# Kernel tuning notes

Hardware: AMD Instinct MI355X
Metric: run time of the kernel (lower is better)

The kernel has to match this reference:

```python
import jax, jax.numpy as jnp
import numpy as np
from jax.ops import segment_sum, segment_max

DIM = 32   # hidden dim (hardcoded in Net)
N = 10000  # nodes
E = 160000 # edges
B = 64     # graphs in batch


def setup_inputs():
    key = jax.random.key(0)
    ks = jax.random.split(key, 16)
    r = lambda k, s: jax.random.normal(k, s, dtype=jnp.float32) * 0.1
    z = lambda s: jnp.zeros(s, jnp.float32)
    return {
        "x": jax.random.normal(ks[0], (N, 1), jnp.float32),
        "edge_attr": jax.random.normal(ks[1], (E, 2), jnp.float32),
        "lin0_w": r(ks[2], (1, DIM)), "lin0_b": z((DIM,)),
        "nn_w1": r(ks[3], (2, 128)), "nn_b1": z((128,)),
        "nn_w2": r(ks[4], (128, DIM * DIM)), "nn_b2": z((DIM * DIM,)),
        "conv_root": r(ks[5], (DIM, DIM)), "conv_bias": z((DIM,)),
        "gru_w_ih": r(ks[6], (DIM, 3 * DIM)), "gru_w_hh": r(ks[7], (DIM, 3 * DIM)),
        "gru_b_ih": z((3 * DIM,)), "gru_b_hh": z((3 * DIM,)),
        "lstm_w_ih": r(ks[8], (2 * DIM, 4 * DIM)), "lstm_w_hh": r(ks[9], (DIM, 4 * DIM)),
        "lstm_b_ih": z((4 * DIM,)), "lstm_b_hh": z((4 * DIM,)),
        "lin1_w": r(ks[10], (2 * DIM, DIM)), "lin1_b": z((DIM,)),
        "lin2_w": r(ks[11], (DIM, 1)), "lin2_b": z((1,)),
        "edge_index": jax.random.randint(ks[12], (2, E), 0, N),
        "batch": jnp.sort(jax.random.randint(ks[13], (N,), 0, B)),
    }


def _forward(x, edge_attr, params, edge_index, batch):
    (lin0_w, lin0_b, nn_w1, nn_b1, nn_w2, nn_b2, conv_root, conv_bias,
     gru_w_ih, gru_w_hh, gru_b_ih, gru_b_hh,
     lstm_w_ih, lstm_w_hh, lstm_b_ih, lstm_b_hh,
     lin1_w, lin1_b, lin2_w, lin2_b) = params
    src, dst = edge_index[0], edge_index[1]
    deg = jnp.maximum(segment_sum(jnp.ones((E,), x.dtype), dst, num_segments=N), 1.0)[:, None]
    # edge-conditioned weight matrices (depend only on edge_attr -> compute once)
    ew = (jax.nn.relu(edge_attr @ nn_w1 + nn_b1) @ nn_w2 + nn_b2).reshape(E, DIM, DIM)

    out = jax.nn.relu(x @ lin0_w + lin0_b)  # (N, DIM)
    h = out                                  # GRU hidden state
    for _ in range(3):
        # NNConv: gather -> per-edge matmul -> scatter-mean, plus root weight + bias
        msg = jnp.einsum('ei,eio->eo', out[src], ew)          # (E, DIM)
        agg = segment_sum(msg, dst, num_segments=N) / deg      # (N, DIM)
        m = jax.nn.relu(agg + out @ conv_root + conv_bias)
        # single GRU step (seq_len = 1)
        gi = m @ gru_w_ih + gru_b_ih
        gh = h @ gru_w_hh + gru_b_hh
        i_r, i_z, i_n = jnp.split(gi, 3, axis=-1)
        h_r, h_z, h_n = jnp.split(gh, 3, axis=-1)
        rg = jax.nn.sigmoid(i_r + h_r)
        zg = jax.nn.sigmoid(i_z + h_z)
        ng = jnp.tanh(i_n + rg * h_n)
        h = (1.0 - zg) * ng + zg * h
        out = h

    # Set2Set pooling, 3 processing steps
    q_star = jnp.zeros((B, 2 * DIM), x.dtype)
    hh = jnp.zeros((B, DIM), x.dtype)
    cc = jnp.zeros((B, DIM), x.dtype)
    for _ in range(3):
        gates = q_star @ lstm_w_ih + lstm_b_ih + hh @ lstm_w_hh + lstm_b_hh
        ig, fg, gg, og = jnp.split(gates, 4, axis=-1)  # torch gate order i,f,g,o
        cc = jax.nn.sigmoid(fg) * cc + jax.nn.sigmoid(ig) * jnp.tanh(gg)
        hh = jax.nn.sigmoid(og) * jnp.tanh(cc)
        q = hh                                          # (B, DIM)
        e = jnp.sum(out * q[batch], axis=-1)            # (N,)
        a = jnp.exp(e - segment_max(e, batch, num_segments=B)[batch])
        a = a / segment_sum(a, batch, num_segments=B)[batch]
        rvec = segment_sum(a[:, None] * out, batch, num_segments=B)  # (B, DIM)
        q_star = jnp.concatenate([q, rvec], axis=-1)

    y = jax.nn.relu(q_star @ lin1_w + lin1_b)
    return (y @ lin2_w + lin2_b).reshape(-1)  # (B,)


def reference(x, edge_attr, lin0_w, lin0_b, nn_w1, nn_b1, nn_w2, nn_b2, conv_root, conv_bias, gru_w_ih, gru_w_hh, gru_b_ih, gru_b_hh, lstm_w_ih, lstm_w_hh, lstm_b_ih, lstm_b_hh, lin1_w, lin1_b, lin2_w, lin2_b, edge_index, batch):
    params = (lin0_w, lin0_b, nn_w1, nn_b1, nn_w2, nn_b2, conv_root, conv_bias,
              gru_w_ih, gru_w_hh, gru_b_ih, gru_b_hh,
              lstm_w_ih, lstm_w_hh, lstm_b_ih, lstm_b_hh,
              lin1_w, lin1_b, lin2_w, lin2_b)
    return _forward(x, edge_attr, params, edge_index, batch)
```

## Files before the change

kernel.cpp:

```cpp
#include <hip/hip_runtime.h>
#include <math.h>

#define NN 10000
#define NE 160000
#define NG 64
#define DIM 32
#define CAP 96

typedef __attribute__((ext_vector_type(8))) short bf16x8;
typedef __attribute__((ext_vector_type(4))) float f32x4;

__device__ __forceinline__ float sigmoidf_(float x) { return 1.f / (1.f + expf(-x)); }

__device__ __forceinline__ unsigned short f2bf(float x) {
    unsigned u = __float_as_uint(x);
    u += 0x7FFF + ((u >> 16) & 1);
    return (unsigned short)(u >> 16);
}
__device__ __forceinline__ float bf2f(unsigned short b) {
    return __uint_as_float(((unsigned)b) << 16);
}

__global__ void k_setup(const float* __restrict__ w2, unsigned short* __restrict__ w2f,
                        const float* __restrict__ x, const float* __restrict__ lw,
                        const float* __restrict__ lb, float* __restrict__ out,
                        const int* __restrict__ batch, int* __restrict__ gstart,
                        const int* __restrict__ ei, const float* __restrict__ ea,
                        int* __restrict__ cursor,
                        int* __restrict__ srt_src, float* __restrict__ srt_ea) {
    int b = blockIdx.x, t = threadIdx.x;
    if (b < 512) {
        int tid = b * 256 + t;
        int h = tid >> 10, rem = tid & 1023, i = rem >> 5, n = rem & 31;
        float v = w2[tid];
        unsigned short hi = f2bf(v);
        unsigned short lo = f2bf(v - bf2f(hi));
        int s = h >> 5, hm = h & 31, q = hm >> 3, j = hm & 7;
        int tile = n >> 4, nn = n & 15, lane = q * 16 + nn;
        int c = (i * 4 + s) * 2 + tile;
        w2f[(c * 2 + 0) * 512 + lane * 8 + j] = hi;
        w2f[(c * 2 + 1) * 512 + lane * 8 + j] = lo;
    } else if (b < 1762) {
        int idx = (b - 512) * 256 + t;
        int n = idx >> 5, d = idx & 31;
        out[idx] = fmaxf(x[n] * lw[d] + lb[d], 0.f);
    } else if (b == 1762) {
        if (t <= NG) {
            int g = t, lo = 0, hi = NN;
            while (lo < hi) { int mid = (lo + hi) >> 1; if (batch[mid] < g) lo = mid + 1; else hi = mid; }
            gstart[g] = lo;
        }
    } else {
        int e = (b - 1763) * 256 + t;
        if (e < NE) {
            int d = ei[NE + e];
            int p = atomicAdd(&cursor[d], 1);
            int pos = d * CAP + p;
            srt_src[pos] = ei[e];
            srt_ea[2 * pos]     = ea[2 * e];
            srt_ea[2 * pos + 1] = ea[2 * e + 1];
        }
    }
}

#define NS 1040
#define PS 8320
__global__ __launch_bounds__(512, 4) void k_conv_gru(
    const int* __restrict__ cursor, const int* __restrict__ srt_src,
    const float* __restrict__ srt_ea,
    const float* __restrict__ w1, const float* __restrict__ b1,
    const unsigned short* __restrict__ w2f, const float* __restrict__ b2,
    const float* __restrict__ out_old,
    float* __restrict__ Sg,
    const float* __restrict__ root, const float* __restrict__ cbias,
    const float* __restrict__ wih, const float* __restrict__ whh,
    const float* __restrict__ bih, const float* __restrict__ bhh,
    float* __restrict__ out_new)
{
    __shared__ __align__(16) unsigned short RB[2 * PS];
    int t = threadIdx.x;
    int wave = t >> 6, lane = t & 63;
    int n0 = blockIdx.x * 8;
    int n = n0 + wave;

    float Racc[64];
    #pragma unroll
    for (int i = 0; i < 64; ++i) Racc[i] = 0.f;
    float sacc = 0.f;

    float w1a0 = w1[lane],      w1c0 = w1[128 + lane],  bb0 = b1[lane];
    float w1a1 = w1[64 + lane], w1c1 = w1[192 + lane],  bb1 = b1[64 + lane];

    int rs = n * CAP;
    int re = rs + cursor[n];
    const float2* eap = (const float2*)srt_ea;

    int p = rs;
    for (; p + 1 < re; p += 2) {
        int s0 = __builtin_amdgcn_readfirstlane(srt_src[p]);
        int s1 = __builtin_amdgcn_readfirstlane(srt_src[p + 1]);
        float2 a0 = eap[p];
        float2 a1 = eap[p + 1];
        const float* o0 = out_old + s0 * DIM;
        const float* o1 = out_old + s1 * DIM;
        float r00 = fmaxf(a0.x * w1a0 + a0.y * w1c0 + bb0, 0.f);
        float r01 = fmaxf(a0.x * w1a1 + a0.y * w1c1 + bb1, 0.f);
        float r10 = fmaxf(a1.x * w1a0 + a1.y * w1c0 + bb0, 0.f);
        float r11 = fmaxf(a1.x * w1a1 + a1.y * w1c1 + bb1, 0.f);
        #pragma unroll
        for (int q = 0; q < 32; ++q) {
            float v0 = o0[q];
            Racc[q]      += r00 * v0;
            Racc[32 + q] += r01 * v0;
        }
        #pragma unroll
        for (int q = 0; q < 32; ++q) {
            float v1 = o1[q];
            Racc[q]      += r10 * v1;
            Racc[32 + q] += r11 * v1;
        }
        if (lane < DIM) sacc += o0[lane] + o1[lane];
    }
    if (p < re) {
        int s0 = __builtin_amdgcn_readfirstlane(srt_src[p]);
        float2 a0 = eap[p];
        const float* o0 = out_old + s0 * DIM;
        float r00 = fmaxf(a0.x * w1a0 + a0.y * w1c0 + bb0, 0.f);
        float r01 = fmaxf(a0.x * w1a1 + a0.y * w1c1 + bb1, 0.f);
        #pragma unroll
        for (int q = 0; q < 32; ++q) {
            float v0 = o0[q];
            Racc[q]      += r00 * v0;
            Racc[32 + q] += r01 * v0;
        }
        if (lane < DIM) sacc += o0[lane];
    }
    if (lane < DIM) Sg[n * DIM + lane] = sacc;

    int quad = lane >> 4;
    int mm = lane & 7;
    unsigned aoff = (unsigned)(mm * NS + wave * 128 + quad * 8);
    f32x4 acc0 = {0.f, 0.f, 0.f, 0.f};
    f32x4 acc1 = {0.f, 0.f, 0.f, 0.f};

    unsigned short* Hw = RB + wave * NS;
    unsigned short* Lw = RB + PS + wave * NS;

    #pragma unroll
    for (int pass = 0; pass < 4; ++pass) {
        if (pass) __syncthreads();
        #pragma unroll
        for (int li = 0; li < 8; ++li) {
            float v0 = Racc[pass * 8 + li];
            float v1 = Racc[32 + pass * 8 + li];
            unsigned short h0 = f2bf(v0);
            unsigned short l0 = f2bf(v0 - bf2f(h0));
            unsigned short h1 = f2bf(v1);
            unsigned short l1 = f2bf(v1 - bf2f(h1));
            Hw[li * 128 + lane] = h0;  Hw[li * 128 + 64 + lane] = h1;
            Lw[li * 128 + lane] = l0;  Lw[li * 128 + 64 + lane] = l1;
        }
        __syncthreads();
        int ig = pass * 8 + wave;
        #pragma unroll
        for (int s = 0; s < 4; ++s) {
            bf16x8 ah = *(const bf16x8*)(RB + aoff + s * 32);
            bf16x8 al = *(const bf16x8*)(RB + PS + aoff + s * 32);
            const unsigned short* bp = w2f + (unsigned)((ig * 4 + s) * 2048 + lane * 8);
            bf16x8 bh0 = *(const bf16x8*)(bp);
            bf16x8 bl0 = *(const bf16x8*)(bp + 512);
            bf16x8 bh1 = *(const bf16x8*)(bp + 1024);
            bf16x8 bl1 = *(const bf16x8*)(bp + 1536);
            acc0 = __builtin_amdgcn_mfma_f32_16x16x32_bf16(ah, bh0, acc0, 0, 0, 0);
            acc0 = __builtin_amdgcn_mfma_f32_16x16x32_bf16(ah, bl0, acc0, 0, 0, 0);
            acc0 = __builtin_amdgcn_mfma_f32_16x16x32_bf16(al, bh0, acc0, 0, 0, 0);
            acc1 = __builtin_amdgcn_mfma_f32_16x16x32_bf16(ah, bh1, acc1, 0, 0, 0);
            acc1 = __builtin_amdgcn_mfma_f32_16x16x32_bf16(ah, bl1, acc1, 0, 0, 0);
            acc1 = __builtin_amdgcn_mfma_f32_16x16x32_bf16(al, bh1, acc1, 0, 0, 0);
        }
    }
    __syncthreads();

    float* part = (float*)RB;
    #pragma unroll
    for (int r = 0; r < 4; ++r) {
        part[((wave * 2 + 0) * 64 + lane) * 4 + r] = acc0[r];
        part[((wave * 2 + 1) * 64 + lane) * 4 + r] = acc1[r];
    }
    __syncthreads();

    if (t < 256) {
        int nb = t >> 5, d = t & 31;
        int nn_ = n0 + nb;
        int base = t & 32;
        int tile = d >> 4, col = d & 15;
        int lidx = (nb >> 2) * 16 + col, reg = nb & 3;
        float aggv = 0.f;
        #pragma unroll
        for (int wv = 0; wv < 8; ++wv)
            aggv += part[((wv * 2 + tile) * 64 + lidx) * 4 + reg];

        float bt = 0.f;
        #pragma unroll 8
        for (int i = 0; i < DIM; ++i) bt += Sg[nn_ * DIM + i] * b2[i * DIM + d];
        int cdeg = cursor[nn_];
        float degf = (float)(cdeg > 0 ? cdeg : 1);
        aggv = (aggv + bt) / degf;

        float x = out_old[nn_ * DIM + d];
        float rootsum = 0.f;
        #pragma unroll 8
        for (int k = 0; k < DIM; ++k)
            rootsum += __shfl(x, base + k) * root[k * DIM + d];
        float m = fmaxf(aggv + rootsum + cbias[d], 0.f);

        float gir = bih[d], giz = bih[DIM + d], gin = bih[2 * DIM + d];
        float ghr = bhh[d], ghz = bhh[DIM + d], ghn = bhh[2 * DIM + d];
        #pragma unroll 4
        for (int k = 0; k < DIM; ++k) {
            float mk = __shfl(m, base + k);
            float hk = __shfl(x, base + k);
            gir += mk * wih[k * 96 + d];
            giz += mk * wih[k * 96 + DIM + d];
            gin += mk * wih[k * 96 + 2 * DIM + d];
            ghr += hk * whh[k * 96 + d];
            ghz += hk * whh[k * 96 + DIM + d];
            ghn += hk * whh[k * 96 + 2 * DIM + d];
        }
        float rg = sigmoidf_(gir + ghr);
        float zg = sigmoidf_(giz + ghz);
        float ng = tanhf(gin + rg * ghn);
        out_new[nn_ * DIM + d] = (1.f - zg) * ng + zg * x;
    }
}

__global__ __launch_bounds__(256) void k_set2set(
    const float* __restrict__ out, const int* __restrict__ gstart,
    const float* __restrict__ wih, const float* __restrict__ whh,
    const float* __restrict__ bih, const float* __restrict__ bhh,
    const float* __restrict__ l1w, const float* __restrict__ l1b,
    const float* __restrict__ l2w, const float* __restrict__ l2b,
    float* __restrict__ ebuf, float* __restrict__ y)
{
    __shared__ float swih[64 * 128];
    __shared__ float swhh[32 * 128];
    __shared__ float sq[2 * DIM];
    __shared__ float shh[DIM], scc[DIM];
    __shared__ float sgates[4 * DIM];
    __shared__ float sacc[8][DIM];
    __shared__ float sredA[4], sredB[4];

    int g = blockIdx.x, t = threadIdx.x;
    {
        const float4* wv = (const float4*)wih;   float4* sv = (float4*)swih;
        for (int i = t; i < 2048; i += 256) sv[i] = wv[i];
        const float4* wv2 = (const float4*)whh;  float4* sv2 = (float4*)swhh;
        for (int i = t; i < 1024; i += 256) sv2[i] = wv2[i];
    }
    if (t < 2 * DIM) sq[t] = 0.f;
    if (t < DIM) { shh[t] = 0.f; scc[t] = 0.f; }
    int ns = gstart[g], ne = gstart[g + 1];
    __syncthreads();

    for (int step = 0; step < 3; ++step) {
        if (t < 128) {
            float acc = bih[t] + bhh[t];
            #pragma unroll 8
            for (int k = 0; k < 2 * DIM; ++k) acc += sq[k] * swih[k * 128 + t];
            #pragma unroll 8
            for (int k = 0; k < DIM; ++k)     acc += shh[k] * swhh[k * 128 + t];
            sgates[t] = acc;
        }
        __syncthreads();
        if (t < DIM) {
            float ig = sigmoidf_(sgates[t]);
            float fg = sigmoidf_(sgates[DIM + t]);
            float gg = tanhf(sgates[2 * DIM + t]);
            float og = sigmoidf_(sgates[3 * DIM + t]);
            float c_new = fg * scc[t] + ig * gg;
            float h_new = og * tanhf(c_new);
            scc[t] = c_new;
            shh[t] = h_new;
            sq[t] = h_new;
        }
        __syncthreads();

        float lmax = -3.0e38f;
        for (int n = ns + t; n < ne; n += 256) {
            const float4* orow = (const float4*)(out + n * DIM);
            float e = 0.f;
            #pragma unroll
            for (int q = 0; q < 8; ++q) {
                float4 o4 = orow[q];
                e += o4.x * shh[4 * q] + o4.y * shh[4 * q + 1]
                   + o4.z * shh[4 * q + 2] + o4.w * shh[4 * q + 3];
            }
            ebuf[n] = e;
            lmax = fmaxf(lmax, e);
        }
        #pragma unroll
        for (int s = 1; s < 64; s <<= 1) lmax = fmaxf(lmax, __shfl_xor(lmax, s));
        if ((t & 63) == 0) sredA[t >> 6] = lmax;
        __syncthreads();
        float M = fmaxf(fmaxf(sredA[0], sredA[1]), fmaxf(sredA[2], sredA[3]));

        float lsum = 0.f;
        for (int n = ns + t; n < ne; n += 256) {
            float v = expf(ebuf[n] - M);
            ebuf[n] = v;
            lsum += v;
        }
        #pragma unroll
        for (int s = 1; s < 64; s <<= 1) lsum += __shfl_xor(lsum, s);
        if ((t & 63) == 0) sredB[t >> 6] = lsum;
        __syncthreads();
        float S = sredB[0] + sredB[1] + sredB[2] + sredB[3];
        float inv = (S > 0.f) ? 1.f / S : 0.f;

        int stp = t >> 5, d = t & 31;
        float racc = 0.f;
        for (int n = ns + stp; n < ne; n += 8)
            racc += ebuf[n] * out[n * DIM + d];
        sacc[stp][d] = racc;
        __syncthreads();
        if (t < DIM) {
            float r = 0.f;
            #pragma unroll
            for (int s = 0; s < 8; ++s) r += sacc[s][t];
            sq[DIM + t] = r * inv;
        }
        __syncthreads();
    }

    if (t < DIM) {
        float h = l1b[t];
        #pragma unroll 8
        for (int k = 0; k < 2 * DIM; ++k) h += sq[k] * l1w[k * DIM + t];
        float v = fmaxf(h, 0.f) * l2w[t];
        #pragma unroll
        for (int s = 1; s < 32; s <<= 1) v += __shfl_xor(v, s);
        if (t == 0) y[g] = v + l2b[0];
    }
}

extern "C" void kernel_launch(void* const* d_in, const int* in_sizes, int n_in,
                              void* d_out, int out_size, void* d_ws, size_t ws_size,
                              hipStream_t stream) {
    const float* x         = (const float*)d_in[0];
    const float* edge_attr = (const float*)d_in[1];
    const float* lin0_w    = (const float*)d_in[2];
    const float* lin0_b    = (const float*)d_in[3];
    const float* nn_w1     = (const float*)d_in[4];
    const float* nn_b1     = (const float*)d_in[5];
    const float* nn_w2     = (const float*)d_in[6];
    const float* nn_b2     = (const float*)d_in[7];
    const float* conv_root = (const float*)d_in[8];
    const float* conv_bias = (const float*)d_in[9];
    const float* gru_w_ih  = (const float*)d_in[10];
    const float* gru_w_hh  = (const float*)d_in[11];
    const float* gru_b_ih  = (const float*)d_in[12];
    const float* gru_b_hh  = (const float*)d_in[13];
    const float* lstm_w_ih = (const float*)d_in[14];
    const float* lstm_w_hh = (const float*)d_in[15];
    const float* lstm_b_ih = (const float*)d_in[16];
    const float* lstm_b_hh = (const float*)d_in[17];
    const float* lin1_w    = (const float*)d_in[18];
    const float* lin1_b    = (const float*)d_in[19];
    const float* lin2_w    = (const float*)d_in[20];
    const float* lin2_b    = (const float*)d_in[21];
    const int*   edge_index= (const int*)d_in[22];
    const int*   batch     = (const int*)d_in[23];
    float* yout = (float*)d_out;

    char* p = (char*)d_ws;
    auto alloc = [&](size_t bytes) { char* r = p; p += (bytes + 255) & ~(size_t)255; return r; };

    int*   cursor = (int*)  alloc(NN * sizeof(int));
    size_t zero_bytes = (size_t)(p - (char*)d_ws);
    int*   gstart    = (int*)  alloc((NG + 1) * sizeof(int));
    int*   srt_src   = (int*)  alloc((size_t)NN * CAP * sizeof(int));
    float* srt_ea    = (float*)alloc((size_t)NN * CAP * 2 * sizeof(float));
    float* outA      = (float*)alloc(NN * DIM * sizeof(float));
    float* outB      = (float*)alloc(NN * DIM * sizeof(float));
    float* Sg        = (float*)alloc(NN * DIM * sizeof(float));
    unsigned short* w2f = (unsigned short*)alloc(262144 * sizeof(unsigned short));
    float* ebuf      = (float*)alloc(NN * sizeof(float));
    (void)ws_size; (void)n_in; (void)in_sizes; (void)out_size;

    hipMemsetAsync(d_ws, 0, zero_bytes, stream);

    k_setup<<<2388, 256, 0, stream>>>(nn_w2, w2f, x, lin0_w, lin0_b, outA, batch, gstart,
                                      edge_index, edge_attr, cursor, srt_src, srt_ea);

    const float* cur = outA;
    float* nxt = outB;
    for (int it = 0; it < 3; ++it) {
        k_conv_gru<<<1250, 512, 0, stream>>>(cursor, srt_src, srt_ea,
                                             nn_w1, nn_b1, w2f, nn_b2,
                                             cur, Sg,
                                             conv_root, conv_bias,
                                             gru_w_ih, gru_w_hh, gru_b_ih, gru_b_hh,
                                             nxt);
        const float* tmp = nxt; nxt = (float*)cur; cur = tmp;
    }
    const float* outF = cur;

    k_set2set<<<NG, 256, 0, stream>>>(outF, gstart,
                                      lstm_w_ih, lstm_w_hh, lstm_b_ih, lstm_b_hh,
                                      lin1_w, lin1_b, lin2_w, lin2_b, ebuf, yout);
}
```

Measured before the change: 327.3 us.

## Split each node's hidden accumulation across two waves, four nodes per block

Each block now handles 4 nodes instead of 8, and two waves share one node, each accumulating half of the 128 hidden units. This halves the per-thread accumulator registers and the shared buffer, which allows a higher launch-bounds occupancy target, and doubles the grid size. In exchange, each neighbor row of out_old is gathered by twice as many waves, and the MFMA tiles now run half-empty (M = 4 rows), so W2 loads are amortized over fewer nodes.

```diff
diff --git a/kernel.cpp b/kernel.cpp
--- a/kernel.cpp
+++ b/kernel.cpp
@@ -64,8 +64,8 @@
 }
 
 #define NS 1040
-#define PS 8320
-__global__ __launch_bounds__(512, 4) void k_conv_gru(
+#define PS 4160
+__global__ __launch_bounds__(512, 6) void k_conv_gru(
     const int* __restrict__ cursor, const int* __restrict__ srt_src,
     const float* __restrict__ srt_ea,
     const float* __restrict__ w1, const float* __restrict__ b1,
@@ -80,19 +80,20 @@
     __shared__ __align__(16) unsigned short RB[2 * PS];
     int t = threadIdx.x;
     int wave = t >> 6, lane = t & 63;
-    int n0 = blockIdx.x * 8;
-    int n = n0 + wave;
-
-    float Racc[64];
+    int n0 = blockIdx.x * 4;
+    int node = n0 + (wave >> 1);
+    int hoff = (wave & 1) * 64;
+
+    float Racc[32];
     #pragma unroll
-    for (int i = 0; i < 64; ++i) Racc[i] = 0.f;
+    for (int i = 0; i < 32; ++i) Racc[i] = 0.f;
     float sacc = 0.f;
 
-    float w1a0 = w1[lane],      w1c0 = w1[128 + lane],  bb0 = b1[lane];
-    float w1a1 = w1[64 + lane], w1c1 = w1[192 + lane],  bb1 = b1[64 + lane];
-
-    int rs = n * CAP;
-    int re = rs + cursor[n];
+    int h = hoff + lane;
+    float w1a = w1[h], w1c = w1[128 + h], bb = b1[h];
+
+    int rs = node * CAP;
+    int re = rs + cursor[node];
     const float2* eap = (const float2*)srt_ea;
 
     int p = rs;
@@ -103,48 +104,33 @@
         float2 a1 = eap[p + 1];
         const float* o0 = out_old + s0 * DIM;
         const float* o1 = out_old + s1 * DIM;
-        float r00 = fmaxf(a0.x * w1a0 + a0.y * w1c0 + bb0, 0.f);
-        float r01 = fmaxf(a0.x * w1a1 + a0.y * w1c1 + bb1, 0.f);
-        float r10 = fmaxf(a1.x * w1a0 + a1.y * w1c0 + bb0, 0.f);
-        float r11 = fmaxf(a1.x * w1a1 + a1.y * w1c1 + bb1, 0.f);
-        #pragma unroll
-        for (int q = 0; q < 32; ++q) {
-            float v0 = o0[q];
-            Racc[q]      += r00 * v0;
-            Racc[32 + q] += r01 * v0;
-        }
-        #pragma unroll
-        for (int q = 0; q < 32; ++q) {
-            float v1 = o1[q];
-            Racc[q]      += r10 * v1;
-            Racc[32 + q] += r11 * v1;
-        }
-        if (lane < DIM) sacc += o0[lane] + o1[lane];
+        float rA = fmaxf(a0.x * w1a + a0.y * w1c + bb, 0.f);
+        float rB = fmaxf(a1.x * w1a + a1.y * w1c + bb, 0.f);
+        #pragma unroll
+        for (int q = 0; q < 32; ++q) Racc[q] += rA * o0[q];
+        #pragma unroll
+        for (int q = 0; q < 32; ++q) Racc[q] += rB * o1[q];
+        if (hoff == 0 && lane < DIM) sacc += o0[lane] + o1[lane];
     }
     if (p < re) {
         int s0 = __builtin_amdgcn_readfirstlane(srt_src[p]);
         float2 a0 = eap[p];
         const float* o0 = out_old + s0 * DIM;
-        float r00 = fmaxf(a0.x * w1a0 + a0.y * w1c0 + bb0, 0.f);
-        float r01 = fmaxf(a0.x * w1a1 + a0.y * w1c1 + bb1, 0.f);
-        #pragma unroll
-        for (int q = 0; q < 32; ++q) {
-            float v0 = o0[q];
-            Racc[q]      += r00 * v0;
-            Racc[32 + q] += r01 * v0;
-        }
-        if (lane < DIM) sacc += o0[lane];
-    }
-    if (lane < DIM) Sg[n * DIM + lane] = sacc;
+        float rA = fmaxf(a0.x * w1a + a0.y * w1c + bb, 0.f);
+        #pragma unroll
+        for (int q = 0; q < 32; ++q) Racc[q] += rA * o0[q];
+        if (hoff == 0 && lane < DIM) sacc += o0[lane];
+    }
+    if (hoff == 0 && lane < DIM) Sg[node * DIM + lane] = sacc;
 
     int quad = lane >> 4;
-    int mm = lane & 7;
+    int mm = lane & 3;
     unsigned aoff = (unsigned)(mm * NS + wave * 128 + quad * 8);
     f32x4 acc0 = {0.f, 0.f, 0.f, 0.f};
     f32x4 acc1 = {0.f, 0.f, 0.f, 0.f};
 
-    unsigned short* Hw = RB + wave * NS;
-    unsigned short* Lw = RB + PS + wave * NS;
+    unsigned short* Hw = RB + (wave >> 1) * NS;
+    unsigned short* Lw = RB + PS + (wave >> 1) * NS;
 
     #pragma unroll
     for (int pass = 0; pass < 4; ++pass) {
@@ -152,13 +138,10 @@
         #pragma unroll
         for (int li = 0; li < 8; ++li) {
             float v0 = Racc[pass * 8 + li];
-            float v1 = Racc[32 + pass * 8 + li];
             unsigned short h0 = f2bf(v0);
             unsigned short l0 = f2bf(v0 - bf2f(h0));
-            unsigned short h1 = f2bf(v1);
-            unsigned short l1 = f2bf(v1 - bf2f(h1));
-            Hw[li * 128 + lane] = h0;  Hw[li * 128 + 64 + lane] = h1;
-            Lw[li * 128 + lane] = l0;  Lw[li * 128 + 64 + lane] = l1;
+            Hw[li * 128 + hoff + lane] = h0;
+            Lw[li * 128 + hoff + lane] = l0;
         }
         __syncthreads();
         int ig = pass * 8 + wave;
@@ -189,16 +172,15 @@
     }
     __syncthreads();
 
-    if (t < 256) {
+    if (t < 128) {
         int nb = t >> 5, d = t & 31;
         int nn_ = n0 + nb;
         int base = t & 32;
         int tile = d >> 4, col = d & 15;
-        int lidx = (nb >> 2) * 16 + col, reg = nb & 3;
         float aggv = 0.f;
         #pragma unroll
         for (int wv = 0; wv < 8; ++wv)
-            aggv += part[((wv * 2 + tile) * 64 + lidx) * 4 + reg];
+            aggv += part[((wv * 2 + tile) * 64 + col) * 4 + nb];
 
         float bt = 0.f;
         #pragma unroll 8
@@ -395,7 +377,7 @@
     const float* cur = outA;
     float* nxt = outB;
     for (int it = 0; it < 3; ++it) {
-        k_conv_gru<<<1250, 512, 0, stream>>>(cursor, srt_src, srt_ea,
+        k_conv_gru<<<2500, 512, 0, stream>>>(cursor, srt_src, srt_ea,
                                              nn_w1, nn_b1, w2f, nn_b2,
                                              cur, Sg,
                                              conv_root, conv_bias,
```

Measured after the change: 384.5 us. +17.5%, slower.
